# Kernel tuning notes

Hardware: AMD Instinct MI355X
Metric: run time of the kernel (lower is better)

Reference implementation:

```python
import jax, jax.numpy as jnp
import numpy as np

N_NODES = 100000
N_EDGES = 3200000
IN_DIM = 256
EMB_DIM = 64
BATCH = 4096
WEIGHT_DECAY = 1e-4


def setup_inputs() -> dict:
    key = jax.random.key(0)
    ks = jax.random.split(key, 8)
    feats = jax.random.normal(ks[0], (N_NODES, IN_DIM), dtype=jnp.float32)
    W = jax.random.normal(ks[1], (IN_DIM, EMB_DIM), dtype=jnp.float32) * (1.0 / np.sqrt(IN_DIM))
    edge_row = jax.random.randint(ks[2], (N_EDGES,), 0, N_NODES, dtype=jnp.int32)
    edge_col = jax.random.randint(ks[3], (N_EDGES,), 0, N_NODES, dtype=jnp.int32)
    edge_val = jax.random.uniform(ks[4], (N_EDGES,), dtype=jnp.float32) * 0.05  # normalized adj weights
    idx1 = jax.random.randint(ks[5], (BATCH,), 0, N_NODES, dtype=jnp.int32)
    idx2 = jax.random.randint(ks[6], (BATCH,), 0, N_NODES, dtype=jnp.int32)
    neg_idx = jax.random.randint(ks[7], (BATCH,), 0, N_NODES, dtype=jnp.int32)
    return {"feats": feats, "W": W, "edge_row": edge_row, "edge_col": edge_col,
            "edge_val": edge_val, "idx1": idx1, "idx2": idx2, "neg_idx": neg_idx}


def reference(feats, W, edge_row, edge_col, edge_val, idx1, idx2, neg_idx):
    # GraphConvolution: tanh( A_sparse @ (X @ W) ), A in COO form
    xw = feats @ W                                              # [N, D]
    msgs = edge_val[:, None] * xw[edge_col]                     # [E, D] gather + scale
    h = jax.ops.segment_sum(msgs, edge_row, num_segments=N_NODES)  # sparse-dense matmul
    h = jnp.tanh(h)
    # tf.nn.l2_normalize(embedding, 1)
    sq = jnp.sum(h * h, axis=1, keepdims=True)
    emb = h * jax.lax.rsqrt(jnp.maximum(sq, 1e-12))             # [N, D]
    # embedding lookups
    o1, o2, on = emb[idx1], emb[idx2], emb[neg_idx]             # [B, D] each
    y_ui = jnp.sum(o1 * o2, axis=1)
    y_uj = jnp.sum(o1 * on, axis=1)
    # BPR loss + weight decay (tf.nn.l2_loss = 0.5*sum(x^2))
    bpr = jnp.sum(-jax.nn.log_sigmoid(y_ui - y_uj))
    loss = (bpr + WEIGHT_DECAY * 0.5 * jnp.sum(emb * emb)) / jnp.float32(BATCH)
    return loss
```

## Files before the change

kernel.cpp:

```cpp
#include <hip/hip_runtime.h>
#include <cmath>

#define N_NODES 100000
#define N_EDGES 3200000
#define IN_DIM 256
#define EMB 64
#define BATCH 4096
#define MWAVES 6250
#define NBUCK 782
#define BROWS 128
#define BSTRIDE 4608
#define PSTRIDE 5504
#define EPB 4096

typedef unsigned long long u64;
typedef unsigned int u32;
typedef unsigned short u16;
typedef __attribute__((ext_vector_type(8))) short bf16x8;
typedef __attribute__((ext_vector_type(4))) float f32x4;

__device__ __forceinline__ float wave_sum(float v) {
#pragma unroll
    for (int m = 1; m < 64; m <<= 1) v += __shfl_xor(v, m, 64);
    return v;
}

__device__ __forceinline__ u16 f2bf_rne(float f) {
    u32 u = __float_as_uint(f);
    u32 r = ((u >> 16) & 1u) + 0x7FFFu;
    return (u16)((u + r) >> 16);
}

__device__ __forceinline__ float bf2f(u32 bits16) {
    return __uint_as_float(bits16 << 16);
}

__global__ __launch_bounds__(256) void mfma_gemm_kernel(const float* __restrict__ feats,
                                                        const float* __restrict__ W,
                                                        u16* __restrict__ xwb) {
    __shared__ u16 wlds[32 * 64 * 8];
    const int tid = threadIdx.x;
    for (int idx = tid; idx < 32 * 64; idx += 256) {
        const int f = idx >> 6, lane = idx & 63;
        const int kt = f >> 2, nt = f & 3;
        const int k0 = kt * 32 + (lane >> 4) * 8;
        const int n  = nt * 16 + (lane & 15);
        u32 buf[4];
#pragma unroll
        for (int jj = 0; jj < 4; ++jj) {
            u16 lo = f2bf_rne(W[(size_t)(k0 + 2 * jj) * EMB + n]);
            u16 hi = f2bf_rne(W[(size_t)(k0 + 2 * jj + 1) * EMB + n]);
            buf[jj] = (u32)lo | ((u32)hi << 16);
        }
        *(uint4*)&wlds[idx * 8] = *(uint4*)buf;
    }
    __syncthreads();

    const int wave = tid >> 6, lane = tid & 63;
    const int wid = blockIdx.x * 4 + wave;
    if (wid >= MWAVES) return;
    const int row0 = wid * 16;
    const int arow = row0 + (lane & 15);
    const int kbase = (lane >> 4) * 8;
    const float* fr = feats + (size_t)arow * IN_DIM + kbase;

    float4 av[16];
#pragma unroll
    for (int kt = 0; kt < 8; ++kt) {
        av[2 * kt]     = *(const float4*)(fr + kt * 32);
        av[2 * kt + 1] = *(const float4*)(fr + kt * 32 + 4);
    }

    f32x4 acc[4] = {};
    const u16* wl = &wlds[lane * 8];
#pragma unroll
    for (int kt = 0; kt < 8; ++kt) {
        float4 a0 = av[2 * kt], a1 = av[2 * kt + 1];
        u32 ab[4];
        ab[0] = (u32)f2bf_rne(a0.x) | ((u32)f2bf_rne(a0.y) << 16);
        ab[1] = (u32)f2bf_rne(a0.z) | ((u32)f2bf_rne(a0.w) << 16);
        ab[2] = (u32)f2bf_rne(a1.x) | ((u32)f2bf_rne(a1.y) << 16);
        ab[3] = (u32)f2bf_rne(a1.z) | ((u32)f2bf_rne(a1.w) << 16);
        bf16x8 afrag = *(bf16x8*)ab;
#pragma unroll
        for (int nt = 0; nt < 4; ++nt) {
            bf16x8 bfrag = *(const bf16x8*)&wl[(kt * 4 + nt) * 512];
            acc[nt] = __builtin_amdgcn_mfma_f32_16x16x32_bf16(afrag, bfrag, acc[nt], 0, 0, 0);
        }
    }
    const int rb = row0 + (lane >> 4) * 4;
    const int cb = lane & 15;
#pragma unroll
    for (int nt = 0; nt < 4; ++nt)
#pragma unroll
        for (int r = 0; r < 4; ++r)
            xwb[(size_t)(rb + r) * EMB + nt * 16 + cb] = f2bf_rne(acc[nt][r]);
}

__global__ __launch_bounds__(256) void passA_kernel(const int* __restrict__ erow,
                                                    const int* __restrict__ ecol,
                                                    const float* __restrict__ eval,
                                                    u32* __restrict__ gcursor,
                                                    u64* __restrict__ sorted) {
    __shared__ u64 stage[EPB];
    __shared__ u32 hist[1024];
    __shared__ u32 offs[1024];
    __shared__ u32 cursor[1024];
    __shared__ u32 gbase[1024];
    __shared__ u32 partial[256];

    const int tid = threadIdx.x;
    const int e0 = blockIdx.x * EPB;
    const int total = min(EPB, N_EDGES - e0);

    for (int i = tid; i < 1024; i += 256) hist[i] = 0;
    __syncthreads();

    u64 ent[16];
    int eb[16];
#pragma unroll
    for (int j = 0; j < 16; ++j) {
        const int e = e0 + j * 256 + tid;
        if (e < N_EDGES) {
            const int r = erow[e];
            const int c = ecol[e];
            const u16 vb = f2bf_rne(eval[e]);
            ent[j] = (u64)(u32)r | ((u64)(u32)c << 17) | ((u64)vb << 34);
            eb[j] = r >> 7;
            atomicAdd(&hist[eb[j]], 1u);
        } else {
            eb[j] = -1;
        }
    }
    __syncthreads();

    u32 local[4], s = 0;
#pragma unroll
    for (int q = 0; q < 4; ++q) {
        local[q] = s;
        s += hist[4 * tid + q];
    }
    partial[tid] = s;
    __syncthreads();
    for (int off = 1; off < 256; off <<= 1) {
        u32 x = (tid >= off) ? partial[tid - off] : 0;
        __syncthreads();
        partial[tid] += x;
        __syncthreads();
    }
    const u32 base = partial[tid] - s;
#pragma unroll
    for (int q = 0; q < 4; ++q) {
        offs[4 * tid + q] = base + local[q];
        cursor[4 * tid + q] = base + local[q];
    }
    __syncthreads();

#pragma unroll
    for (int j = 0; j < 16; ++j) {
        if (eb[j] >= 0) {
            u32 pos = atomicAdd(&cursor[eb[j]], 1u);
            stage[pos] = ent[j];
        }
    }
    __syncthreads();

    for (int b = tid; b < 1024; b += 256) {
        const u32 cnt = cursor[b] - offs[b];
        gbase[b] = cnt ? atomicAdd(&gcursor[b], cnt) : 0;
    }
    __syncthreads();

    for (int i = tid; i < total; i += 256) {
        const u64 p = stage[i];
        const int b = (int)(p & 0x1FFFFu) >> 7;
        const u32 gpos = gbase[b] + ((u32)i - offs[b]);
        if (gpos < BSTRIDE) sorted[(size_t)b * BSTRIDE + gpos] = p;
    }
}

__global__ __launch_bounds__(512, 4) void gather_kernel(const u16* __restrict__ xwb,
                                                        u64* __restrict__ sorted,
                                                        const u32* __restrict__ gcursor,
                                                        float* __restrict__ accumA) {
    __shared__ u32 scoff[PSTRIDE];
    __shared__ u16 sval[PSTRIDE];
    __shared__ u32 rhist[BROWS], roff[BROWS], rcur[BROWS], sc[BROWS];
    __shared__ float part[8];
    const int tid = threadIdx.x, wave = tid >> 6, lane = tid & 63;
    const int b = blockIdx.x;
    u64* gbase = sorted + (size_t)b * BSTRIDE;
    const int cnt = min((int)gcursor[b], BSTRIDE);

    if (tid < BROWS) rhist[tid] = 0;
    __syncthreads();

    u64 ent[9];
    int nloc = 0;
    for (int i = tid; i < cnt; i += 512) {
        u64 p = gbase[i];
        ent[nloc++] = p;
        atomicAdd(&rhist[(int)(p & 127u)], 1u);
    }
    __syncthreads();

    if (tid < BROWS) sc[tid] = (rhist[tid] + 7u) & ~7u;
    __syncthreads();
    for (int off = 1; off < BROWS; off <<= 1) {
        u32 x = (tid < BROWS && tid >= off) ? sc[tid - off] : 0;
        __syncthreads();
        if (tid < BROWS) sc[tid] += x;
        __syncthreads();
    }
    if (tid < BROWS) {
        const u32 r0 = sc[tid] - ((rhist[tid] + 7u) & ~7u);
        roff[tid] = r0;
        rcur[tid] = r0;
    }
    __syncthreads();

    for (int j = 0; j < nloc; ++j) {
        const u64 p = ent[j];
        const u32 pos = atomicAdd(&rcur[(int)(p & 127u)], 1u);
        scoff[pos] = (((u32)(p >> 17)) & 0x1FFFFu) << 7;
        sval[pos]  = (u16)(p >> 34);
    }
    __syncthreads();

    if (tid < BROWS) {
        const int e = roff[tid] + rhist[tid];
        const int pe = roff[tid] + (int)((rhist[tid] + 7u) & ~7u);
        for (int k = e; k < pe; ++k) { scoff[k] = 0u; sval[k] = 0; }
    }
    __syncthreads();

    u16* embp = (u16*)gbase;
    const int g = lane >> 3;
    const int eoff = (lane & 7) * 16;
    const int g0 = g & 1, g1 = (g >> 1) & 1, g2 = (g >> 2) & 1;
    const int el = (lane & 7) * 8 + 4 * g0 + 2 * g1 + g2;
    const char* xwc = (const char*)xwb;
    float wd = 0.f;

#define FMA8(X, V)                                         \
    acc[0] += (V) * __uint_as_float((X).x << 16);          \
    acc[1] += (V) * __uint_as_float((X).x & 0xFFFF0000u);  \
    acc[2] += (V) * __uint_as_float((X).y << 16);          \
    acc[3] += (V) * __uint_as_float((X).y & 0xFFFF0000u);  \
    acc[4] += (V) * __uint_as_float((X).z << 16);          \
    acc[5] += (V) * __uint_as_float((X).z & 0xFFFF0000u);  \
    acc[6] += (V) * __uint_as_float((X).w << 16);          \
    acc[7] += (V) * __uint_as_float((X).w & 0xFFFF0000u);

    for (int rr = 0; rr < 16; ++rr) {
        const int r = wave * 16 + rr;
        const int n8 = (int)((rhist[r] + 7u) & ~7u);
        const int base = (int)roff[r];
        float acc[8] = {0.f, 0.f, 0.f, 0.f, 0.f, 0.f, 0.f, 0.f};

        int j = 0;
        for (; j + 16 <= n8; j += 16) {
            const int i0 = base + j + g;
            const u32 c0 = scoff[i0];
            const u32 c1 = scoff[i0 + 8];
            const float v0 = bf2f(sval[i0]);
            const float v1 = bf2f(sval[i0 + 8]);
            const uint4 x0 = *(const uint4*)(xwc + (c0 + eoff));
            const uint4 x1 = *(const uint4*)(xwc + (c1 + eoff));
            FMA8(x0, v0)
            FMA8(x1, v1)
        }
        if (j < n8) {
            const int i0 = base + j + g;
            const u32 c0 = scoff[i0];
            const float v0 = bf2f(sval[i0]);
            const uint4 x0 = *(const uint4*)(xwc + (c0 + eoff));
            FMA8(x0, v0)
        }

        float k4[4];
#pragma unroll
        for (int i = 0; i < 4; ++i) {
            const float snd = g0 ? acc[i] : acc[i + 4];
            const float kp  = g0 ? acc[i + 4] : acc[i];
            k4[i] = kp + __shfl_xor(snd, 8, 64);
        }
        float k2[2];
#pragma unroll
        for (int i = 0; i < 2; ++i) {
            const float snd = g1 ? k4[i] : k4[i + 2];
            const float kp  = g1 ? k4[i + 2] : k4[i];
            k2[i] = kp + __shfl_xor(snd, 16, 64);
        }
        const float snd = g2 ? k2[0] : k2[1];
        const float kp  = g2 ? k2[1] : k2[0];
        const float s = kp + __shfl_xor(snd, 32, 64);

        const float t = tanhf(s);
        const float sq = wave_sum(t * t);
        const float rn = rsqrtf(fmaxf(sq, 1e-12f));
        if (b * BROWS + r < N_NODES)
            embp[r * EMB + el] = f2bf_rne(t * rn);
        wd += sq / fmaxf(sq, 1e-12f);
    }
#undef FMA8
    if (lane == 0) part[wave] = wd;
    __syncthreads();
    if (tid == 0) {
        float v = 0.f;
#pragma unroll
        for (int w = 0; w < 8; ++w) v += part[w];
        unsafeAtomicAdd(&accumA[b & 255], v);
    }
}

__device__ __forceinline__ float emb_ld(const u64* __restrict__ sorted, int row, int lane) {
    const u16* rp = (const u16*)(sorted + (size_t)(row >> 7) * BSTRIDE) + (row & 127) * EMB;
    return bf2f(rp[lane]);
}

__global__ __launch_bounds__(256) void bpr_kernel(const u64* __restrict__ sorted,
                                                  const int* __restrict__ idx1,
                                                  const int* __restrict__ idx2,
                                                  const int* __restrict__ nidx,
                                                  float* __restrict__ accumB) {
    const int wave = threadIdx.x >> 6, lane = threadIdx.x & 63;
    const int i = blockIdx.x * 4 + wave;
    float o1 = emb_ld(sorted, idx1[i], lane);
    float o2 = emb_ld(sorted, idx2[i], lane);
    float on = emb_ld(sorted, nidx[i], lane);
    float yui = wave_sum(o1 * o2);
    float yuj = wave_sum(o1 * on);
    if (lane == 0) {
        float x = yui - yuj;
        float li = (x > 0.f) ? log1pf(expf(-x)) : (-x + log1pf(expf(x)));
        unsafeAtomicAdd(&accumB[i & 255], li);
    }
}

__global__ __launch_bounds__(64) void finalize_kernel(const float* __restrict__ accumA,
                                                      const float* __restrict__ accumB,
                                                      float* __restrict__ out) {
    const int t = threadIdx.x;
    float wd = 0.f, bp = 0.f;
#pragma unroll
    for (int k = 0; k < 4; ++k) {
        wd += accumA[t + 64 * k];
        bp += accumB[t + 64 * k];
    }
    wd = wave_sum(wd);
    bp = wave_sum(bp);
    if (t == 0) out[0] = (bp + 1e-4f * 0.5f * wd) / (float)BATCH;
}

extern "C" void kernel_launch(void* const* d_in, const int* in_sizes, int n_in,
                              void* d_out, int out_size, void* d_ws, size_t ws_size,
                              hipStream_t stream) {
    const float* feats = (const float*)d_in[0];
    const float* W     = (const float*)d_in[1];
    const int*   erow  = (const int*)d_in[2];
    const int*   ecol  = (const int*)d_in[3];
    const float* eval  = (const float*)d_in[4];
    const int*   idx1  = (const int*)d_in[5];
    const int*   idx2  = (const int*)d_in[6];
    const int*   nidx  = (const int*)d_in[7];
    float* out = (float*)d_out;

    u16*   xwb     = (u16*)d_ws;
    u64*   sorted  = (u64*)(xwb + (size_t)N_NODES * EMB);
    u32*   gcursor = (u32*)(sorted + (size_t)NBUCK * BSTRIDE);
    float* accumA  = (float*)(gcursor + 1024);
    float* accumB  = accumA + 256;

    hipMemsetAsync(gcursor, 0, (1024 + 512) * sizeof(u32), stream);

    mfma_gemm_kernel<<<(MWAVES + 3) / 4, 256, 0, stream>>>(feats, W, xwb);
    passA_kernel<<<(N_EDGES + EPB - 1) / EPB, 256, 0, stream>>>(erow, ecol, eval, gcursor, sorted);
    gather_kernel<<<NBUCK, 512, 0, stream>>>(xwb, sorted, gcursor, accumA);
    bpr_kernel<<<BATCH / 4, 256, 0, stream>>>(sorted, idx1, idx2, nidx, accumB);
    finalize_kernel<<<1, 64, 0, stream>>>(accumA, accumB, out);
}
```

Before: 314.4 us.

## Pre-pack W once and restructure edge bucketing into fewer larger blocks

Adds a small kernel that converts W to bf16 in MFMA fragment layout once, so every GEMM block copies it instead of each block redoing the conversion from fp32. The edge bucketing pass now uses 256 blocks of 1024 threads, each handling 12544 edges, with one bucket per thread and a single 1024-wide scan. This cuts the number of global atomics on bucket cursors and the per-block prefix overhead, but each block uses about 100KB of LDS, which limits occupancy, and it adds one extra kernel launch.

```diff
diff --git a/kernel.cpp b/kernel.cpp
--- a/kernel.cpp
+++ b/kernel.cpp
@@ -11,7 +11,8 @@
 #define BROWS 128
 #define BSTRIDE 4608
 #define PSTRIDE 5504
-#define EPB 4096
+#define EPB 12544
+#define NPA 256
 
 typedef unsigned long long u64;
 typedef unsigned int u32;
@@ -35,25 +36,30 @@
     return __uint_as_float(bits16 << 16);
 }
 
+__global__ __launch_bounds__(256) void wpack_kernel(const float* __restrict__ W,
+                                                    u16* __restrict__ wpack) {
+    const int idx = blockIdx.x * 256 + threadIdx.x;
+    const int f = idx >> 6, lane = idx & 63;
+    const int kt = f >> 2, nt = f & 3;
+    const int k0 = kt * 32 + (lane >> 4) * 8;
+    const int n  = nt * 16 + (lane & 15);
+    u32 buf[4];
+#pragma unroll
+    for (int jj = 0; jj < 4; ++jj) {
+        u16 lo = f2bf_rne(W[(size_t)(k0 + 2 * jj) * EMB + n]);
+        u16 hi = f2bf_rne(W[(size_t)(k0 + 2 * jj + 1) * EMB + n]);
+        buf[jj] = (u32)lo | ((u32)hi << 16);
+    }
+    *(uint4*)&wpack[idx * 8] = *(uint4*)buf;
+}
+
 __global__ __launch_bounds__(256) void mfma_gemm_kernel(const float* __restrict__ feats,
-                                                        const float* __restrict__ W,
+                                                        const u16* __restrict__ wpack,
                                                         u16* __restrict__ xwb) {
     __shared__ u16 wlds[32 * 64 * 8];
     const int tid = threadIdx.x;
-    for (int idx = tid; idx < 32 * 64; idx += 256) {
-        const int f = idx >> 6, lane = idx & 63;
-        const int kt = f >> 2, nt = f & 3;
-        const int k0 = kt * 32 + (lane >> 4) * 8;
-        const int n  = nt * 16 + (lane & 15);
-        u32 buf[4];
-#pragma unroll
-        for (int jj = 0; jj < 4; ++jj) {
-            u16 lo = f2bf_rne(W[(size_t)(k0 + 2 * jj) * EMB + n]);
-            u16 hi = f2bf_rne(W[(size_t)(k0 + 2 * jj + 1) * EMB + n]);
-            buf[jj] = (u32)lo | ((u32)hi << 16);
-        }
-        *(uint4*)&wlds[idx * 8] = *(uint4*)buf;
-    }
+    for (int idx = tid; idx < 32 * 64; idx += 256)
+        *(uint4*)&wlds[idx * 8] = *(const uint4*)&wpack[idx * 8];
     __syncthreads();
 
     const int wave = tid >> 6, lane = tid & 63;
@@ -97,85 +103,71 @@
             xwb[(size_t)(rb + r) * EMB + nt * 16 + cb] = f2bf_rne(acc[nt][r]);
 }
 
-__global__ __launch_bounds__(256) void passA_kernel(const int* __restrict__ erow,
-                                                    const int* __restrict__ ecol,
-                                                    const float* __restrict__ eval,
-                                                    u32* __restrict__ gcursor,
-                                                    u64* __restrict__ sorted) {
+__global__ __launch_bounds__(1024, 4) void passA_kernel(const int* __restrict__ erow,
+                                                        const int* __restrict__ ecol,
+                                                        const float* __restrict__ eval,
+                                                        u32* __restrict__ gcursor,
+                                                        u64* __restrict__ sorted) {
     __shared__ u64 stage[EPB];
     __shared__ u32 hist[1024];
-    __shared__ u32 offs[1024];
+    __shared__ u32 harr[1024];
     __shared__ u32 cursor[1024];
     __shared__ u32 gbase[1024];
-    __shared__ u32 partial[256];
 
     const int tid = threadIdx.x;
     const int e0 = blockIdx.x * EPB;
     const int total = min(EPB, N_EDGES - e0);
 
-    for (int i = tid; i < 1024; i += 256) hist[i] = 0;
-    __syncthreads();
-
-    u64 ent[16];
-    int eb[16];
-#pragma unroll
-    for (int j = 0; j < 16; ++j) {
-        const int e = e0 + j * 256 + tid;
-        if (e < N_EDGES) {
+    hist[tid] = 0;
+    __syncthreads();
+
+    u64 ent[13];
+#pragma unroll
+    for (int j = 0; j < 13; ++j) {
+        const int le = j * 1024 + tid;
+        if (le < total) {
+            const int e = e0 + le;
             const int r = erow[e];
             const int c = ecol[e];
             const u16 vb = f2bf_rne(eval[e]);
             ent[j] = (u64)(u32)r | ((u64)(u32)c << 17) | ((u64)vb << 34);
-            eb[j] = r >> 7;
-            atomicAdd(&hist[eb[j]], 1u);
-        } else {
-            eb[j] = -1;
-        }
-    }
-    __syncthreads();
-
-    u32 local[4], s = 0;
-#pragma unroll
-    for (int q = 0; q < 4; ++q) {
-        local[q] = s;
-        s += hist[4 * tid + q];
-    }
-    partial[tid] = s;
-    __syncthreads();
-    for (int off = 1; off < 256; off <<= 1) {
-        u32 x = (tid >= off) ? partial[tid - off] : 0;
+            atomicAdd(&hist[r >> 7], 1u);
+        }
+    }
+    __syncthreads();
+
+    const u32 h = hist[tid];
+    harr[tid] = h;
+    __syncthreads();
+    for (int off = 1; off < 1024; off <<= 1) {
+        u32 x = (tid >= off) ? harr[tid - off] : 0;
         __syncthreads();
-        partial[tid] += x;
+        harr[tid] += x;
         __syncthreads();
     }
-    const u32 base = partial[tid] - s;
-#pragma unroll
-    for (int q = 0; q < 4; ++q) {
-        offs[4 * tid + q] = base + local[q];
-        cursor[4 * tid + q] = base + local[q];
-    }
-    __syncthreads();
-
-#pragma unroll
-    for (int j = 0; j < 16; ++j) {
-        if (eb[j] >= 0) {
-            u32 pos = atomicAdd(&cursor[eb[j]], 1u);
-            stage[pos] = ent[j];
-        }
-    }
-    __syncthreads();
-
-    for (int b = tid; b < 1024; b += 256) {
-        const u32 cnt = cursor[b] - offs[b];
-        gbase[b] = cnt ? atomicAdd(&gcursor[b], cnt) : 0;
-    }
-    __syncthreads();
-
-    for (int i = tid; i < total; i += 256) {
+    const u32 myoff = harr[tid] - h;
+    __syncthreads();
+    harr[tid] = myoff;
+    cursor[tid] = myoff;
+    gbase[tid] = h ? atomicAdd(&gcursor[tid], h) : 0u;
+    __syncthreads();
+
+#pragma unroll
+    for (int j = 0; j < 13; ++j) {
+        const int le = j * 1024 + tid;
+        if (le < total) {
+            const u64 p = ent[j];
+            const u32 pos = atomicAdd(&cursor[(int)(p & 0x1FFFFu) >> 7], 1u);
+            stage[pos] = p;
+        }
+    }
+    __syncthreads();
+
+    for (int i = tid; i < total; i += 1024) {
         const u64 p = stage[i];
-        const int b = (int)(p & 0x1FFFFu) >> 7;
-        const u32 gpos = gbase[b] + ((u32)i - offs[b]);
-        if (gpos < BSTRIDE) sorted[(size_t)b * BSTRIDE + gpos] = p;
+        const int bk = (int)(p & 0x1FFFFu) >> 7;
+        const u32 gpos = gbase[bk] + ((u32)i - harr[bk]);
+        if (gpos < BSTRIDE) sorted[(size_t)bk * BSTRIDE + gpos] = p;
     }
 }
 
@@ -371,11 +363,13 @@
     u32*   gcursor = (u32*)(sorted + (size_t)NBUCK * BSTRIDE);
     float* accumA  = (float*)(gcursor + 1024);
     float* accumB  = accumA + 256;
+    u16*   wpack   = (u16*)(accumB + 256);
 
     hipMemsetAsync(gcursor, 0, (1024 + 512) * sizeof(u32), stream);
 
-    mfma_gemm_kernel<<<(MWAVES + 3) / 4, 256, 0, stream>>>(feats, W, xwb);
-    passA_kernel<<<(N_EDGES + EPB - 1) / EPB, 256, 0, stream>>>(erow, ecol, eval, gcursor, sorted);
+    wpack_kernel<<<8, 256, 0, stream>>>(W, wpack);
+    mfma_gemm_kernel<<<(MWAVES + 3) / 4, 256, 0, stream>>>(feats, wpack, xwb);
+    passA_kernel<<<NPA, 1024, 0, stream>>>(erow, ecol, eval, gcursor, sorted);
     gather_kernel<<<NBUCK, 512, 0, stream>>>(xwb, sorted, gcursor, accumA);
     bpr_kernel<<<BATCH / 4, 256, 0, stream>>>(sorted, idx1, idx2, nidx, accumB);
     finalize_kernel<<<1, 64, 0, stream>>>(accumA, accumB, out);
```

Measured after the change: 280.1 us. 10.9% less time.
